# Kernel optimization log

Measured on AMD Instinct MI355X. Metric: run time of the kernel, lower is better.

The kernel has to match this reference:

```python
import jax, jax.numpy as jnp
import numpy as np

H = 128
R = 14
B = 2048
TYPES = ['operator', 'table', 'column', 'predicate', 'operation', 'literal', 'numeral']
SIZES = {'operator': 100000, 'table': 20000, 'column': 120000, 'predicate': 60000,
         'operation': 100000, 'literal': 50000, 'numeral': 50000}
FEAT = {'operator': 4, 'table': 2, 'column': 10, 'predicate': 4, 'operation': 8,
        'literal': 1, 'numeral': 1}
# (name, src_type, dst_type, num_edges), order matches edge_type_mapping in the torch module
EDGES = [('ei_scannedby', 'table', 'operator', 100000),
         ('ei_pred_filters', 'predicate', 'operator', 100000),
         ('ei_outputby', 'column', 'operator', 100000),
         ('ei_col_connects', 'column', 'operation', 100000),
         ('ei_calledby', 'operator', 'operator', 100000),
         ('ei_op_filters', 'operation', 'operator', 100000),
         ('ei_op_connects', 'operation', 'predicate', 100000),
         ('ei_lit_connects', 'literal', 'operation', 100000),
         ('ei_num_connects', 'numeral', 'operation', 100000),
         ('ei_lit_self', 'literal', 'literal', 50000),
         ('ei_num_self', 'numeral', 'numeral', 50000),
         ('ei_tab_self', 'table', 'table', 20000),
         ('ei_col_self', 'column', 'column', 120000),
         ('ei_pred_self', 'predicate', 'predicate', 60000)]
OFFS = {}
_o = 0
for _t in TYPES:
    OFFS[_t] = _o
    _o += SIZES[_t]
N_TOTAL = _o


def setup_inputs():
    key = jax.random.key(0)
    ks = iter(jax.random.split(key, 64))
    inp = {}
    for t in TYPES:
        inp['x_' + t] = jax.random.normal(next(ks), (SIZES[t], FEAT[t]), jnp.float32)
    for name, s, d, E in EDGES:
        src = jax.random.randint(next(ks), (E,), 0, SIZES[s], jnp.int32)
        dst = jax.random.randint(next(ks), (E,), 0, SIZES[d], jnp.int32)
        inp[name] = jnp.stack([src, dst])
    inp['batch_operator'] = jnp.sort(
        jax.random.randint(next(ks), (SIZES['operator'],), 0, B, jnp.int32))

    def lin_w(k, din, dout):
        s = 1.0 / float(np.sqrt(din))
        return jax.random.uniform(k, (din, dout), jnp.float32, -s, s)

    for t in TYPES:
        inp['W_' + t] = lin_w(next(ks), FEAT[t], H)
        inp['b_' + t] = jnp.zeros((H,), jnp.float32)
    for c in ('c1', 'c2'):
        inp[c + '_root'] = lin_w(next(ks), H, H)
        inp[c + '_rel'] = jax.random.normal(next(ks), (R, H, H), jnp.float32) / float(np.sqrt(H))
        inp[c + '_bias'] = jnp.zeros((H,), jnp.float32)
    inp['n1_g'] = jnp.ones((H,), jnp.float32); inp['n1_b'] = jnp.zeros((H,), jnp.float32)
    inp['n2_g'] = jnp.ones((H,), jnp.float32); inp['n2_b'] = jnp.zeros((H,), jnp.float32)
    inp['W_lin'] = lin_w(next(ks), H, 1)
    inp['b_lin'] = jnp.zeros((1,), jnp.float32)
    return inp


def layer_norm(x, g, b, eps=1e-5):
    mu = jnp.mean(x, axis=-1, keepdims=True)
    var = jnp.var(x, axis=-1, keepdims=True)
    return (x - mu) * jax.lax.rsqrt(var + eps) * g + b


def rgcn(x, rel_edges, w_root, w_rel, bias):
    # PyG RGCNConv: root transform + per-relation gather -> GEMM -> scatter-mean into dst
    out = x @ w_root
    for r, (src, dst) in enumerate(rel_edges):
        msg = x[src] @ w_rel[r]  # [E_r, H]
        agg = jax.ops.segment_sum(msg, dst, num_segments=N_TOTAL)
        cnt = jax.ops.segment_sum(jnp.ones(src.shape, x.dtype), dst, num_segments=N_TOTAL)
        out = out + agg / jnp.maximum(cnt, 1.0)[:, None]
    return out + bias


def reference(x_operator, x_table, x_column, x_predicate, x_operation, x_literal, x_numeral,
              ei_scannedby, ei_pred_filters, ei_outputby, ei_col_connects, ei_calledby,
              ei_op_filters, ei_op_connects, ei_lit_connects, ei_num_connects, ei_lit_self,
              ei_num_self, ei_tab_self, ei_col_self, ei_pred_self, batch_operator,
              W_operator, b_operator, W_table, b_table, W_column, b_column,
              W_predicate, b_predicate, W_operation, b_operation, W_literal, b_literal,
              W_numeral, b_numeral, c1_root, c1_rel, c1_bias, c2_root, c2_rel, c2_bias,
              n1_g, n1_b, n2_g, n2_b, W_lin, b_lin):
    # per-node-type input embedding, then concat in fixed type order
    x = jnp.concatenate([
        x_operator @ W_operator + b_operator,
        x_table @ W_table + b_table,
        x_column @ W_column + b_column,
        x_predicate @ W_predicate + b_predicate,
        x_operation @ W_operation + b_operation,
        x_literal @ W_literal + b_literal,
        x_numeral @ W_numeral + b_numeral], axis=0)
    eis = [ei_scannedby, ei_pred_filters, ei_outputby, ei_col_connects, ei_calledby,
           ei_op_filters, ei_op_connects, ei_lit_connects, ei_num_connects, ei_lit_self,
           ei_num_self, ei_tab_self, ei_col_self, ei_pred_self]
    rel_edges = [(e[0] + OFFS[s], e[1] + OFFS[d]) for e, (_, s, d, _) in zip(eis, EDGES)]
    h = rgcn(x, rel_edges, c1_root, c1_rel, c1_bias)
    h = layer_norm(jax.nn.elu(h), n1_g, n1_b)  # dropout is identity in eval mode
    h = rgcn(h, rel_edges, c2_root, c2_rel, c2_bias)
    h = layer_norm(jax.nn.elu(h), n2_g, n2_b)
    op = h[:SIZES['operator']]  # operator offset is 0
    cnt = jax.ops.segment_sum(jnp.ones((op.shape[0],), op.dtype), batch_operator, num_segments=B)
    pooled = jax.ops.segment_sum(op, batch_operator, num_segments=B) / jnp.maximum(cnt, 1.0)[:, None]
    return (pooled @ W_lin + b_lin)[:, 0]  # [B]
```

## Files before the change

kernel.cpp:

```cpp
#include <hip/hip_runtime.h>
#include <hip/hip_bf16.h>
#include <math.h>

#define HD 128
#define N_OP 100000
#define N_L1 400000
#define NB 2048
#define CNT_TOT 1160000
#define EDG_TOT 1100000

typedef short short8 __attribute__((ext_vector_type(8)));
typedef float floatx4 __attribute__((ext_vector_type(4)));

static const int REL_E[14]    = {100000,100000,100000,100000,100000,100000,100000,100000,100000,50000,50000,20000,120000,60000};
static const int REL_DSZ[14]  = {100000,100000,100000,100000,100000,100000,60000,100000,100000,50000,50000,20000,120000,60000};
static const int CNT_OFF[14]  = {0,100000,200000,300000,400000,500000,600000,660000,760000,860000,910000,960000,980000,1100000};
static const int SRC_T[14] = {1,3,2,2,0,4,4,5,6,5,6,1,2,3};
static const int TF[7]  = {4,2,10,4,8,1,1};
static const size_t AGR_OFF[14] = {0,200000,600000,1600000,2600000,3000000,3800000,4280000,4380000,0,0,4480000,4520000,5720000};
#define AGR_TOT 5960000
static const int RELW[14] = {4,7,12,93,23,28,70,104,106,-1,-1,40,54,79};
static const int RELI[14] = {6,11,22,103,27,36,78,105,107,-1,-1,42,64,83};
static const int ROOTW[5] = {0,38,44,66,85};
static const int ROOTB[5] = {37,43,65,84,108};
#define WL1_ROWS 109

__device__ inline unsigned short f2bf(float f) {
  union { float f; unsigned int u; } v; v.f = f;
  unsigned int r = v.u + 0x7FFF + ((v.u >> 16) & 1);
  return (unsigned short)(r >> 16);
}
__device__ inline float bfu2f(unsigned short u) {
  union { unsigned int i; float f; } v; v.i = ((unsigned int)u) << 16; return v.f;
}

struct CJob { const int* dst; int coff; int E; int blk0; };
struct CPackK { CJob j[12]; int bblk0; const int* batch; float* pcnt; int nop; };

__global__ void count_k(CPackK P, int* __restrict__ ICNT) {
  int b = blockIdx.x;
  if (b >= P.bblk0) {
    int i = (b - P.bblk0) * 256 + threadIdx.x;
    if (i < P.nop) atomicAdd(&P.pcnt[P.batch[i]], 1.0f);
    return;
  }
  int ji = 0;
#pragma unroll
  for (int i = 1; i < 12; ++i) if (b >= P.j[i].blk0) ji = i;
  CJob J = P.j[ji];
  int e = (b - J.blk0) * 256 + threadIdx.x;
  if (e < J.E) atomicAdd(&ICNT[J.coff + J.dst[e]], 1);
}

#define SCAN_BLK 1024
__global__ void scan1(const int* __restrict__ in, int* __restrict__ out,
                      int* __restrict__ bsum, int n) {
  __shared__ int sh[256];
  int t = threadIdx.x;
  int base = blockIdx.x * SCAN_BLK + t * 4;
  int v0 = 0, v1 = 0, v2 = 0, v3 = 0;
  if (base + 3 < n) { int4 q = *(const int4*)&in[base]; v0 = q.x; v1 = q.y; v2 = q.z; v3 = q.w; }
  else {
    if (base < n) v0 = in[base];
    if (base + 1 < n) v1 = in[base + 1];
    if (base + 2 < n) v2 = in[base + 2];
    if (base + 3 < n) v3 = in[base + 3];
  }
  int ts = v0 + v1 + v2 + v3;
  sh[t] = ts; __syncthreads();
  for (int o = 1; o < 256; o <<= 1) {
    int x = (t >= o) ? sh[t - o] : 0;
    __syncthreads();
    sh[t] += x;
    __syncthreads();
  }
  int excl = sh[t] - ts;
  if (base < n) out[base] = excl;
  if (base + 1 < n) out[base + 1] = excl + v0;
  if (base + 2 < n) out[base + 2] = excl + v0 + v1;
  if (base + 3 < n) out[base + 3] = excl + v0 + v1 + v2;
  if (t == 255) bsum[blockIdx.x] = sh[255];
}

__global__ void scan2(int* __restrict__ bs, int nb) {
  __shared__ int sh[256];
  int t = threadIdx.x;
  const int C = 5;
  int v[C]; int ts = 0;
#pragma unroll
  for (int i = 0; i < C; ++i) { int idx = t * C + i; v[i] = (idx < nb) ? bs[idx] : 0; ts += v[i]; }
  sh[t] = ts; __syncthreads();
  for (int o = 1; o < 256; o <<= 1) {
    int x = (t >= o) ? sh[t - o] : 0;
    __syncthreads();
    sh[t] += x;
    __syncthreads();
  }
  int run = sh[t] - ts;
#pragma unroll
  for (int i = 0; i < C; ++i) { int idx = t * C + i; if (idx < nb) bs[idx] = run; run += v[i]; }
}

__global__ void scan3(int* __restrict__ CUR, int2* __restrict__ OFF2,
                      const int* __restrict__ ICNT, const int* __restrict__ bs, int n) {
  int i = blockIdx.x * 256 + threadIdx.x;
  if (i < n) {
    int o = CUR[i] + bs[i >> 10];
    CUR[i] = o;
    OFF2[i] = make_int2(o, ICNT[i]);
  }
}

struct FJob { const int* src; const int* dst; int coff; int E; int blk0; };
struct FPackK { FJob j[12]; };

__global__ void fill_k(FPackK P, int* __restrict__ CUR, int* __restrict__ EDG) {
  int b = blockIdx.x;
  int ji = 0;
#pragma unroll
  for (int i = 1; i < 12; ++i) if (b >= P.j[i].blk0) ji = i;
  FJob J = P.j[ji];
  int e = (b - J.blk0) * 256 + threadIdx.x;
  if (e < J.E) {
    int pos = atomicAdd(&CUR[J.coff + J.dst[e]], 1);
    EDG[pos] = J.src[e];
  }
}

struct GJob { const float* x; float* agr; int coff; int D; int F; int blk0; };
struct GPack { GJob j[12]; };

template <int F>
__device__ inline void gathF(const float* __restrict__ x, float* __restrict__ agr,
                             const int* __restrict__ EDG, int2 oc, int d) {
  if (oc.y == 0) return;
  float s[F];
#pragma unroll
  for (int f = 0; f < F; ++f) s[f] = 0.f;
  for (int e = 0; e < oc.y; ++e) {
    int si = EDG[oc.x + e];
    const float* xp = &x[(size_t)si * F];
#pragma unroll
    for (int f = 0; f < F; ++f) s[f] += xp[f];
  }
  float rc = 1.0f / (float)oc.y;
  float* ap = &agr[(size_t)d * F];
#pragma unroll
  for (int f = 0; f < F; ++f) ap[f] = s[f] * rc;
}

__global__ void gather_all(GPack P, const int2* __restrict__ OFF2, const int* __restrict__ EDG) {
  int b = blockIdx.x;
  int ji = 0;
#pragma unroll
  for (int i = 1; i < 12; ++i) if (b >= P.j[i].blk0) ji = i;
  GJob J = P.j[ji];
  int d = (b - J.blk0) * 256 + threadIdx.x;
  if (d >= J.D) return;
  int2 oc = OFF2[J.coff + d];
  switch (J.F) {
    case 1:  gathF<1>(J.x, J.agr, EDG, oc, d); break;
    case 2:  gathF<2>(J.x, J.agr, EDG, oc, d); break;
    case 4:  gathF<4>(J.x, J.agr, EDG, oc, d); break;
    case 8:  gathF<8>(J.x, J.agr, EDG, oc, d); break;
    default: gathF<10>(J.x, J.agr, EDG, oc, d); break;
  }
}

struct CombJob { const float* A; const float* bin; const float* Mtx; const float* extra; float* Wout; float* bout; int F; };
struct CombPack { CombJob j[17]; };

__global__ void weights_prep(CombPack P, const float* __restrict__ c2root,
                             const float* __restrict__ c2rel, __hip_bfloat16* __restrict__ Wt) {
  int b = blockIdx.x;
  if (b < 17) {
    if (threadIdx.x >= 128) return;
    CombJob J = P.j[b];
    int c = threadIdx.x;
    for (int f = 0; f <= J.F; ++f) {
      const float* arow = (f < J.F) ? &J.A[f * HD] : J.bin;
      float s = (f < J.F) ? 0.f : (J.extra ? J.extra[c] : 0.f);
      for (int k = 0; k < HD; ++k) s = fmaf(arow[k], J.Mtx[k * HD + c], s);
      if (f < J.F) J.Wout[f * HD + c] = s;
      else J.bout[c] = s;
    }
  } else {
    const int RID[6] = {-1, 0, 1, 2, 4, 5};
    int j = b - 17;
    const float* W = (j == 0) ? c2root : (c2rel + (size_t)RID[j] * HD * HD);
    __hip_bfloat16* o = Wt + (size_t)j * HD * 136;
    for (int i = threadIdx.x; i < HD * HD; i += 256) {
      int k = i >> 7, n = i & 127;
      o[n * 136 + k] = __float2bfloat16(W[i]);
    }
  }
}

struct L1v2 {
  const float* x0; const float* x1; const float* x2; const float* x3; const float* x4;
  const float* AGR; const float* WL1; const int2* OFF2;
  const float* g; const float* b;
  unsigned short* Hb;
};

template <int F>
__device__ inline void ld_rel(float* s, const float* __restrict__ agr,
                              const int2* __restrict__ OFF2, int cb, int row) {
  int cnt = OFF2[cb + row].y;
  if (cnt > 0) {
    const float* ap = &agr[(size_t)row * F];
#pragma unroll
    for (int f = 0; f < F; ++f) s[f] = ap[f];
    s[F] = 1.f;
  } else {
#pragma unroll
    for (int f = 0; f <= F; ++f) s[f] = 0.f;
  }
}

template <int KT>
__device__ inline float2 l1_dot(const float* __restrict__ Ls, const float (&s)[KT], int c2) {
  float2 a;
  a.x = Ls[KT * 128 + c2];
  a.y = Ls[KT * 128 + c2 + 1];
#pragma unroll
  for (int k = 0; k < KT; ++k) {
    a.x = fmaf(s[k], Ls[k * 128 + c2], a.x);
    a.y = fmaf(s[k], Ls[k * 128 + c2 + 1], a.y);
  }
  return a;
}

__device__ inline void l1_fin(float2 a, int c2, const float* __restrict__ g,
                              const float* __restrict__ bb,
                              unsigned short* __restrict__ Hb, int orow) {
  a.x = (a.x > 0.f) ? a.x : (expf(a.x) - 1.f);
  a.y = (a.y > 0.f) ? a.y : (expf(a.y) - 1.f);
  float s = a.x + a.y, sq = a.x * a.x + a.y * a.y;
#pragma unroll
  for (int m = 32; m >= 1; m >>= 1) {
    s += __shfl_xor(s, m, 64);
    sq += __shfl_xor(sq, m, 64);
  }
  float mean = s * (1.0f / HD);
  float var = sq * (1.0f / HD) - mean * mean;
  float rstd = rsqrtf(var + 1e-5f);
  float2 gg = *(const float2*)&g[c2];
  float2 b2 = *(const float2*)&bb[c2];
  float ox = (a.x - mean) * rstd * gg.x + b2.x;
  float oy = (a.y - mean) * rstd * gg.y + b2.y;
  unsigned int pack = (unsigned int)f2bf(ox) | ((unsigned int)f2bf(oy) << 16);
  *(unsigned int*)&Hb[(size_t)orow * HD + c2] = pack;
}

__global__ __launch_bounds__(256) void layer1_v2(L1v2 A) {
  __shared__ float Ls[38 * 128];
  const int b = blockIdx.x, t = threadIdx.x;
  const int wv = t >> 6, lane = t & 63, c2 = lane * 2;
  int type, seg;
  if (b < 391) { type = 0; seg = b; }
  else if (b < 470) { type = 1; seg = b - 391; }
  else if (b < 939) { type = 2; seg = b - 470; }
  else if (b < 1174) { type = 3; seg = b - 939; }
  else { type = 4; seg = b - 1174; }
  const int NR[5] = {38, 6, 22, 19, 24};
  const int RB[5] = {0, 38, 44, 66, 85};
  const int TR[5] = {100000, 20000, 120000, 60000, 100000};
  const int OB[5] = {0, 100000, 120000, 240000, 300000};
  {
    const float4* src = (const float4*)(A.WL1 + RB[type] * 128);
    float4* dst = (float4*)Ls;
    int n4 = NR[type] * 32;
    for (int i = t; i < n4; i += 256) dst[i] = src[i];
  }
  __syncthreads();
  const int row0 = seg * 256, M = TR[type], ob = OB[type];

  if (type == 0) {
    for (int it = 0; it < 64; ++it) {
      int row = row0 + it * 4 + wv;
      if (row >= M) break;
      float s[37];
      const float* xp = &A.x0[(size_t)row * 4];
#pragma unroll
      for (int f = 0; f < 4; ++f) s[f] = xp[f];
      ld_rel<2>(s + 4, A.AGR + 0, A.OFF2, 0, row);
      ld_rel<4>(s + 7, A.AGR + 200000, A.OFF2, 100000, row);
      ld_rel<10>(s + 12, A.AGR + 600000, A.OFF2, 200000, row);
      ld_rel<4>(s + 23, A.AGR + 2600000, A.OFF2, 400000, row);
      ld_rel<8>(s + 28, A.AGR + 3000000, A.OFF2, 500000, row);
      l1_fin(l1_dot<37>(Ls, s, c2), c2, A.g, A.b, A.Hb, ob + row);
    }
  } else if (type == 1) {
    for (int it = 0; it < 64; ++it) {
      int row = row0 + it * 4 + wv;
      if (row >= M) break;
      float s[5];
      const float* xp = &A.x1[(size_t)row * 2];
#pragma unroll
      for (int f = 0; f < 2; ++f) s[f] = xp[f];
      ld_rel<2>(s + 2, A.AGR + 4480000, A.OFF2, 960000, row);
      l1_fin(l1_dot<5>(Ls, s, c2), c2, A.g, A.b, A.Hb, ob + row);
    }
  } else if (type == 2) {
    for (int it = 0; it < 64; ++it) {
      int row = row0 + it * 4 + wv;
      if (row >= M) break;
      float s[21];
      const float* xp = &A.x2[(size_t)row * 10];
#pragma unroll
      for (int f = 0; f < 10; ++f) s[f] = xp[f];
      ld_rel<10>(s + 10, A.AGR + 4520000, A.OFF2, 980000, row);
      l1_fin(l1_dot<21>(Ls, s, c2), c2, A.g, A.b, A.Hb, ob + row);
    }
  } else if (type == 3) {
    for (int it = 0; it < 64; ++it) {
      int row = row0 + it * 4 + wv;
      if (row >= M) break;
      float s[18];
      const float* xp = &A.x3[(size_t)row * 4];
#pragma unroll
      for (int f = 0; f < 4; ++f) s[f] = xp[f];
      ld_rel<8>(s + 4, A.AGR + 3800000, A.OFF2, 600000, row);
      ld_rel<4>(s + 13, A.AGR + 5720000, A.OFF2, 1100000, row);
      l1_fin(l1_dot<18>(Ls, s, c2), c2, A.g, A.b, A.Hb, ob + row);
    }
  } else {
    for (int it = 0; it < 64; ++it) {
      int row = row0 + it * 4 + wv;
      if (row >= M) break;
      float s[23];
      const float* xp = &A.x4[(size_t)row * 8];
#pragma unroll
      for (int f = 0; f < 8; ++f) s[f] = xp[f];
      ld_rel<10>(s + 8, A.AGR + 1600000, A.OFF2, 300000, row);
      ld_rel<1>(s + 19, A.AGR + 4280000, A.OFF2, 660000, row);
      ld_rel<1>(s + 21, A.AGR + 4380000, A.OFF2, 760000, row);
      l1_fin(l1_dot<23>(Ls, s, c2), c2, A.g, A.b, A.Hb, ob + row);
    }
  }
}

__global__ __launch_bounds__(256, 4)
void l2_fused(const unsigned short* __restrict__ Hb, const unsigned short* __restrict__ Wall,
              const int2* __restrict__ OFF2, const int* __restrict__ EDG,
              const float* __restrict__ c2bias, const float* __restrict__ n2g,
              const float* __restrict__ n2b, const float* __restrict__ Wl,
              const int* __restrict__ batch, float* __restrict__ accb, int M) {
  const int CSR_OFF[5] = {0, 100000, 200000, 400000, 500000};
  const int SOFF[5]    = {100000, 240000, 120000, 0, 300000};
  __shared__ unsigned short Ws[128 * 136];
  const int t = threadIdx.x, wv = t >> 6, ln = t & 63;
  const int quad = ln >> 4, ln15 = ln & 15, q8 = quad * 8;
  const int m0 = blockIdx.x * 64;
  const int rowA = m0 + wv * 16 + ln15;

  float bias_c[8], gw[8];
  float pg = 0.f, pb = 0.f;
#pragma unroll
  for (int nt = 0; nt < 8; ++nt) {
    int col = nt * 16 + ln15;
    float wl = Wl[col], gc = n2g[col], bc = n2b[col];
    bias_c[nt] = c2bias[col];
    gw[nt] = gc * wl;
    pg += gc * wl;
    pb += bc * wl;
  }
#pragma unroll
  for (int m = 8; m >= 1; m >>= 1) {
    pg += __shfl_xor(pg, m, 64);
    pb += __shfl_xor(pb, m, 64);
  }

  floatx4 acc[8];
#pragma unroll
  for (int b = 0; b < 8; ++b) acc[b] = (floatx4){0.f, 0.f, 0.f, 0.f};

  for (int term = 0; term < 6; ++term) {
    __syncthreads();
    {
      const uint4* wg = (const uint4*)(Wall + (size_t)term * 128 * 136);
      uint4* ws4 = (uint4*)Ws;
#pragma unroll
      for (int i = 0; i < 9; ++i) {
        int idx = i * 256 + t;
        if (idx < 2176) ws4[idx] = wg[idx];
      }
    }
    __syncthreads();

    short8 afr[4];
    if (term == 0) {
      if (rowA < M) {
#pragma unroll
        for (int k4 = 0; k4 < 4; ++k4)
          afr[k4] = *(const short8*)&Hb[(size_t)rowA * HD + k4 * 32 + q8];
      } else {
#pragma unroll
        for (int k4 = 0; k4 < 4; ++k4)
#pragma unroll
          for (int j = 0; j < 8; ++j) afr[k4][j] = 0;
      }
    } else {
      float sum[4][8];
#pragma unroll
      for (int k4 = 0; k4 < 4; ++k4)
#pragma unroll
        for (int j = 0; j < 8; ++j) sum[k4][j] = 0.f;
      if (rowA < M) {
        int2 oc = OFF2[CSR_OFF[term - 1] + rowA];
        if (oc.y > 0) {
          int so = SOFF[term - 1];
          for (int e = 0; e < oc.y; ++e) {
            size_t s = (size_t)(EDG[oc.x + e] + so);
#pragma unroll
            for (int k4 = 0; k4 < 4; ++k4) {
              short8 h = *(const short8*)&Hb[s * HD + k4 * 32 + q8];
#pragma unroll
              for (int j = 0; j < 8; ++j) sum[k4][j] += bfu2f((unsigned short)h[j]);
            }
          }
          float rc = 1.0f / (float)oc.y;
#pragma unroll
          for (int k4 = 0; k4 < 4; ++k4)
#pragma unroll
            for (int j = 0; j < 8; ++j) sum[k4][j] *= rc;
        }
      }
#pragma unroll
      for (int k4 = 0; k4 < 4; ++k4)
#pragma unroll
        for (int j = 0; j < 8; ++j) afr[k4][j] = (short)f2bf(sum[k4][j]);
    }

#pragma unroll
    for (int nt = 0; nt < 8; ++nt) {
      int wrow = nt * 16 + ln15;
      short8 b0 = *(const short8*)&Ws[wrow * 136 + 0 + q8];
      short8 b1 = *(const short8*)&Ws[wrow * 136 + 32 + q8];
      short8 b2 = *(const short8*)&Ws[wrow * 136 + 64 + q8];
      short8 b3 = *(const short8*)&Ws[wrow * 136 + 96 + q8];
      acc[nt] = __builtin_amdgcn_mfma_f32_16x16x32_bf16(afr[0], b0, acc[nt], 0, 0, 0);
      acc[nt] = __builtin_amdgcn_mfma_f32_16x16x32_bf16(afr[1], b1, acc[nt], 0, 0, 0);
      acc[nt] = __builtin_amdgcn_mfma_f32_16x16x32_bf16(afr[2], b2, acc[nt], 0, 0, 0);
      acc[nt] = __builtin_amdgcn_mfma_f32_16x16x32_bf16(afr[3], b3, acc[nt], 0, 0, 0);
    }
  }

#pragma unroll
  for (int r = 0; r < 4; ++r) {
    int rowD = m0 + wv * 16 + quad * 4 + r;
    float p = 0.f, q = 0.f, s1 = 0.f;
#pragma unroll
    for (int nt = 0; nt < 8; ++nt) {
      float v = acc[nt][r] + bias_c[nt];
      float e = (v > 0.f) ? v : (expf(v) - 1.f);
      p += e; q += e * e; s1 += e * gw[nt];
    }
#pragma unroll
    for (int m = 8; m >= 1; m >>= 1) {
      p += __shfl_xor(p, m, 64);
      q += __shfl_xor(q, m, 64);
      s1 += __shfl_xor(s1, m, 64);
    }
    if (ln15 == 0 && rowD < M) {
      float mean = p * (1.0f / HD);
      float var = q * (1.0f / HD) - mean * mean;
      float rstd = rsqrtf(var + 1e-5f);
      float o = rstd * (s1 - mean * pg) + pb;
      atomicAdd(&accb[batch[rowD]], o);
    }
  }
}

__global__ void final_kernel(const float* __restrict__ accb, const float* __restrict__ pcnt,
                             const float* __restrict__ bl, float* __restrict__ out) {
  int b = blockIdx.x * 256 + threadIdx.x;
  if (b < NB) out[b] = accb[b] / fmaxf(pcnt[b], 1.0f) + bl[0];
}

extern "C" void kernel_launch(void* const* d_in, const int* in_sizes, int n_in,
                              void* d_out, int out_size, void* d_ws, size_t ws_size,
                              hipStream_t stream) {
  const float* xt[7];
  for (int t = 0; t < 7; ++t) xt[t] = (const float*)d_in[t];
  const int* ei[14];
  for (int r = 0; r < 14; ++r) ei[r] = (const int*)d_in[7 + r];
  const int* batch = (const int*)d_in[21];
  const float* Wemb[7]; const float* bemb[7];
  for (int t = 0; t < 7; ++t) { Wemb[t] = (const float*)d_in[22 + 2 * t]; bemb[t] = (const float*)d_in[23 + 2 * t]; }
  const float* c_root[2] = {(const float*)d_in[36], (const float*)d_in[39]};
  const float* c_rel[2]  = {(const float*)d_in[37], (const float*)d_in[40]};
  const float* c_bias[2] = {(const float*)d_in[38], (const float*)d_in[41]};
  const float* ng[2] = {(const float*)d_in[42], (const float*)d_in[44]};
  const float* nbv[2] = {(const float*)d_in[43], (const float*)d_in[45]};
  const float* Wlin = (const float*)d_in[46];
  const float* blin = (const float*)d_in[47];
  float* out = (float*)d_out;

  char* base = (char*)d_ws;
  size_t off = 0;
  auto alloc = [&](size_t bytes) -> void* {
    void* p = base + off;
    off += (bytes + 255) & ~(size_t)255;
    return p;
  };
  __hip_bfloat16* Hb = (__hip_bfloat16*)alloc((size_t)N_L1 * HD * 2);
  float* AGR  = (float*)alloc((size_t)AGR_TOT * 4);
  int*   ICNT = (int*)alloc((size_t)CNT_TOT * 4);
  int*   CUR  = (int*)alloc((size_t)CNT_TOT * 4);
  int2*  OFF2 = (int2*)alloc((size_t)CNT_TOT * 8);
  int*   EDG  = (int*)alloc((size_t)EDG_TOT * 4);
  int*   BS   = (int*)alloc((size_t)1152 * 4);
  float* WL1  = (float*)alloc((size_t)WL1_ROWS * 128 * 4);
  __hip_bfloat16* WT2 = (__hip_bfloat16*)alloc((size_t)6 * HD * 136 * 2);
  float* ACC  = (float*)alloc((size_t)NB * 4);
  float* PCNT = (float*)alloc((size_t)NB * 4);

  static const int l1_rels[12] = {0,1,2,3,4,5,6,7,8,11,12,13};

  hipMemsetAsync(ICNT, 0, (size_t)CNT_TOT * 4, stream);
  hipMemsetAsync(ACC, 0, (size_t)2 * NB * 4, stream);

  CPackK CP1;
  int blk = 0;
  for (int q = 0; q < 12; ++q) {
    int r = l1_rels[q];
    CP1.j[q].dst = ei[r] + REL_E[r];
    CP1.j[q].coff = CNT_OFF[r];
    CP1.j[q].E = REL_E[r];
    CP1.j[q].blk0 = blk;
    blk += (REL_E[r] + 255) / 256;
  }
  CP1.bblk0 = blk; CP1.batch = batch; CP1.pcnt = PCNT; CP1.nop = N_OP;
  blk += (N_OP + 255) / 256;
  count_k<<<blk, 256, 0, stream>>>(CP1, ICNT);

  int nb1 = (CNT_TOT + SCAN_BLK - 1) / SCAN_BLK;
  scan1<<<nb1, 256, 0, stream>>>(ICNT, CUR, BS, CNT_TOT);
  scan2<<<1, 256, 0, stream>>>(BS, nb1);
  scan3<<<(CNT_TOT + 255) / 256, 256, 0, stream>>>(CUR, OFF2, ICNT, BS, CNT_TOT);

  FPackK FP;
  blk = 0;
  for (int q = 0; q < 12; ++q) {
    int r = l1_rels[q];
    FP.j[q].src = ei[r];
    FP.j[q].dst = ei[r] + REL_E[r];
    FP.j[q].coff = CNT_OFF[r];
    FP.j[q].E = REL_E[r];
    FP.j[q].blk0 = blk;
    blk += (REL_E[r] + 255) / 256;
  }
  fill_k<<<blk, 256, 0, stream>>>(FP, CUR, EDG);

  CombPack CP;
  for (int q = 0; q < 12; ++q) {
    int r = l1_rels[q]; int t = SRC_T[r];
    CombJob& J = CP.j[q];
    J.A = Wemb[t]; J.bin = bemb[t]; J.Mtx = c_rel[0] + (size_t)r * HD * HD;
    J.extra = nullptr;
    J.Wout = WL1 + (size_t)RELW[r] * 128;
    J.bout = WL1 + (size_t)RELI[r] * 128;
    J.F = TF[t];
  }
  for (int t = 0; t < 5; ++t) {
    CombJob& J = CP.j[12 + t];
    J.A = Wemb[t]; J.bin = bemb[t]; J.Mtx = c_root[0];
    J.extra = c_bias[0];
    J.Wout = WL1 + (size_t)ROOTW[t] * 128;
    J.bout = WL1 + (size_t)ROOTB[t] * 128;
    J.F = TF[t];
  }
  weights_prep<<<23, 256, 0, stream>>>(CP, c_root[1], c_rel[1], WT2);

  GPack GP;
  blk = 0;
  for (int q = 0; q < 12; ++q) {
    int r = l1_rels[q]; int t = SRC_T[r];
    GP.j[q].x = xt[t];
    GP.j[q].agr = AGR + AGR_OFF[r];
    GP.j[q].coff = CNT_OFF[r];
    GP.j[q].D = REL_DSZ[r];
    GP.j[q].F = TF[t];
    GP.j[q].blk0 = blk;
    blk += (REL_DSZ[r] + 255) / 256;
  }
  gather_all<<<blk, 256, 0, stream>>>(GP, OFF2, EDG);

  L1v2 A;
  A.x0 = xt[0]; A.x1 = xt[1]; A.x2 = xt[2]; A.x3 = xt[3]; A.x4 = xt[4];
  A.AGR = AGR; A.WL1 = WL1; A.OFF2 = OFF2;
  A.g = ng[0]; A.b = nbv[0]; A.Hb = (unsigned short*)Hb;
  layer1_v2<<<1565, 256, 0, stream>>>(A);

  l2_fused<<<(N_OP + 63) / 64, 256, 0, stream>>>(
      (const unsigned short*)Hb, (const unsigned short*)WT2,
      OFF2, EDG, c_bias[1], ng[1], nbv[1], Wlin, batch, ACC, N_OP);

  final_kernel<<<(NB + 255) / 256, 256, 0, stream>>>(ACC, PCNT, blin, out);
}
```

Before: 677.6 us.

## Remap layer1 so each 16-lane group handles one row with 8 columns per lane

Rewrites the layer-1 dense+ELU+LayerNorm kernel so each wave processes four rows at once, each row split across 16 lanes that each own 8 contiguous columns. It uses float4 LDS weight reads and a uint4 bf16 store, and shortens the shuffle reduction to 4 steps. Rows per block drop from 256 to 64, so the grid grows from 1565 to 6252 blocks. The aim is more memory-level parallelism on the per-row gathers and fewer LDS and shuffle instructions, at the cost of more registers per thread and the weight staging being repeated across more blocks.

```diff
diff --git a/kernel.cpp b/kernel.cpp
--- a/kernel.cpp
+++ b/kernel.cpp
@@ -219,50 +219,68 @@
 }
 
 template <int KT>
-__device__ inline float2 l1_dot(const float* __restrict__ Ls, const float (&s)[KT], int c2) {
-  float2 a;
-  a.x = Ls[KT * 128 + c2];
-  a.y = Ls[KT * 128 + c2 + 1];
+__device__ inline void l1_dot8(const float* __restrict__ Ls, const float (&s)[KT],
+                               int c8, float (&a)[8]) {
+  {
+    float4 w0 = *(const float4*)&Ls[KT * 128 + c8];
+    float4 w1 = *(const float4*)&Ls[KT * 128 + c8 + 4];
+    a[0] = w0.x; a[1] = w0.y; a[2] = w0.z; a[3] = w0.w;
+    a[4] = w1.x; a[5] = w1.y; a[6] = w1.z; a[7] = w1.w;
+  }
 #pragma unroll
   for (int k = 0; k < KT; ++k) {
-    a.x = fmaf(s[k], Ls[k * 128 + c2], a.x);
-    a.y = fmaf(s[k], Ls[k * 128 + c2 + 1], a.y);
-  }
-  return a;
-}
-
-__device__ inline void l1_fin(float2 a, int c2, const float* __restrict__ g,
-                              const float* __restrict__ bb,
-                              unsigned short* __restrict__ Hb, int orow) {
-  a.x = (a.x > 0.f) ? a.x : (expf(a.x) - 1.f);
-  a.y = (a.y > 0.f) ? a.y : (expf(a.y) - 1.f);
-  float s = a.x + a.y, sq = a.x * a.x + a.y * a.y;
-#pragma unroll
-  for (int m = 32; m >= 1; m >>= 1) {
-    s += __shfl_xor(s, m, 64);
-    sq += __shfl_xor(sq, m, 64);
-  }
-  float mean = s * (1.0f / HD);
-  float var = sq * (1.0f / HD) - mean * mean;
+    float4 w0 = *(const float4*)&Ls[k * 128 + c8];
+    float4 w1 = *(const float4*)&Ls[k * 128 + c8 + 4];
+    a[0] = fmaf(s[k], w0.x, a[0]); a[1] = fmaf(s[k], w0.y, a[1]);
+    a[2] = fmaf(s[k], w0.z, a[2]); a[3] = fmaf(s[k], w0.w, a[3]);
+    a[4] = fmaf(s[k], w1.x, a[4]); a[5] = fmaf(s[k], w1.y, a[5]);
+    a[6] = fmaf(s[k], w1.z, a[6]); a[7] = fmaf(s[k], w1.w, a[7]);
+  }
+}
+
+__device__ inline void l1_fin8(float (&a)[8], int c8, const float* __restrict__ g,
+                               const float* __restrict__ bb,
+                               unsigned short* __restrict__ Hb, int orow) {
+  float p = 0.f, q = 0.f;
+#pragma unroll
+  for (int j = 0; j < 8; ++j) {
+    a[j] = (a[j] > 0.f) ? a[j] : (expf(a[j]) - 1.f);
+    p += a[j]; q += a[j] * a[j];
+  }
+#pragma unroll
+  for (int m = 8; m >= 1; m >>= 1) {
+    p += __shfl_xor(p, m, 64);
+    q += __shfl_xor(q, m, 64);
+  }
+  float mean = p * (1.0f / HD);
+  float var = q * (1.0f / HD) - mean * mean;
   float rstd = rsqrtf(var + 1e-5f);
-  float2 gg = *(const float2*)&g[c2];
-  float2 b2 = *(const float2*)&bb[c2];
-  float ox = (a.x - mean) * rstd * gg.x + b2.x;
-  float oy = (a.y - mean) * rstd * gg.y + b2.y;
-  unsigned int pack = (unsigned int)f2bf(ox) | ((unsigned int)f2bf(oy) << 16);
-  *(unsigned int*)&Hb[(size_t)orow * HD + c2] = pack;
-}
-
-__global__ __launch_bounds__(256) void layer1_v2(L1v2 A) {
+  float4 g0 = *(const float4*)&g[c8], g1 = *(const float4*)&g[c8 + 4];
+  float4 b0 = *(const float4*)&bb[c8], b1 = *(const float4*)&bb[c8 + 4];
+  float gg[8] = {g0.x, g0.y, g0.z, g0.w, g1.x, g1.y, g1.z, g1.w};
+  float bv[8] = {b0.x, b0.y, b0.z, b0.w, b1.x, b1.y, b1.z, b1.w};
+  unsigned int pk[4];
+#pragma unroll
+  for (int j = 0; j < 4; ++j) {
+    float o0 = (a[2 * j] - mean) * rstd * gg[2 * j] + bv[2 * j];
+    float o1 = (a[2 * j + 1] - mean) * rstd * gg[2 * j + 1] + bv[2 * j + 1];
+    pk[j] = (unsigned int)f2bf(o0) | ((unsigned int)f2bf(o1) << 16);
+  }
+  uint4 st; st.x = pk[0]; st.y = pk[1]; st.z = pk[2]; st.w = pk[3];
+  *(uint4*)&Hb[(size_t)orow * HD + c8] = st;
+}
+
+__global__ __launch_bounds__(256) void layer1_v3(L1v2 A) {
   __shared__ float Ls[38 * 128];
   const int b = blockIdx.x, t = threadIdx.x;
-  const int wv = t >> 6, lane = t & 63, c2 = lane * 2;
+  const int wv = t >> 6, ln = t & 63;
+  const int sub = ln >> 4, c8 = (ln & 15) * 8;
   int type, seg;
-  if (b < 391) { type = 0; seg = b; }
-  else if (b < 470) { type = 1; seg = b - 391; }
-  else if (b < 939) { type = 2; seg = b - 470; }
-  else if (b < 1174) { type = 3; seg = b - 939; }
-  else { type = 4; seg = b - 1174; }
+  if (b < 1563) { type = 0; seg = b; }
+  else if (b < 1876) { type = 1; seg = b - 1563; }
+  else if (b < 3751) { type = 2; seg = b - 1876; }
+  else if (b < 4689) { type = 3; seg = b - 3751; }
+  else { type = 4; seg = b - 4689; }
   const int NR[5] = {38, 6, 22, 19, 24};
   const int RB[5] = {0, 38, 44, 66, 85};
   const int TR[5] = {100000, 20000, 120000, 60000, 100000};
@@ -274,12 +292,13 @@
     for (int i = t; i < n4; i += 256) dst[i] = src[i];
   }
   __syncthreads();
-  const int row0 = seg * 256, M = TR[type], ob = OB[type];
+  const int row0 = seg * 64, M = TR[type], ob = OB[type];
 
   if (type == 0) {
-    for (int it = 0; it < 64; ++it) {
-      int row = row0 + it * 4 + wv;
-      if (row >= M) break;
+#pragma unroll
+    for (int it = 0; it < 4; ++it) {
+      int row = row0 + it * 16 + wv * 4 + sub;
+      if (row >= M) continue;
       float s[37];
       const float* xp = &A.x0[(size_t)row * 4];
 #pragma unroll
@@ -289,46 +308,58 @@
       ld_rel<10>(s + 12, A.AGR + 600000, A.OFF2, 200000, row);
       ld_rel<4>(s + 23, A.AGR + 2600000, A.OFF2, 400000, row);
       ld_rel<8>(s + 28, A.AGR + 3000000, A.OFF2, 500000, row);
-      l1_fin(l1_dot<37>(Ls, s, c2), c2, A.g, A.b, A.Hb, ob + row);
+      float a[8];
+      l1_dot8<37>(Ls, s, c8, a);
+      l1_fin8(a, c8, A.g, A.b, A.Hb, ob + row);
     }
   } else if (type == 1) {
-    for (int it = 0; it < 64; ++it) {
-      int row = row0 + it * 4 + wv;
-      if (row >= M) break;
+#pragma unroll
+    for (int it = 0; it < 4; ++it) {
+      int row = row0 + it * 16 + wv * 4 + sub;
+      if (row >= M) continue;
       float s[5];
       const float* xp = &A.x1[(size_t)row * 2];
 #pragma unroll
       for (int f = 0; f < 2; ++f) s[f] = xp[f];
       ld_rel<2>(s + 2, A.AGR + 4480000, A.OFF2, 960000, row);
-      l1_fin(l1_dot<5>(Ls, s, c2), c2, A.g, A.b, A.Hb, ob + row);
+      float a[8];
+      l1_dot8<5>(Ls, s, c8, a);
+      l1_fin8(a, c8, A.g, A.b, A.Hb, ob + row);
     }
   } else if (type == 2) {
-    for (int it = 0; it < 64; ++it) {
-      int row = row0 + it * 4 + wv;
-      if (row >= M) break;
+#pragma unroll
+    for (int it = 0; it < 4; ++it) {
+      int row = row0 + it * 16 + wv * 4 + sub;
+      if (row >= M) continue;
       float s[21];
       const float* xp = &A.x2[(size_t)row * 10];
 #pragma unroll
       for (int f = 0; f < 10; ++f) s[f] = xp[f];
       ld_rel<10>(s + 10, A.AGR + 4520000, A.OFF2, 980000, row);
-      l1_fin(l1_dot<21>(Ls, s, c2), c2, A.g, A.b, A.Hb, ob + row);
+      float a[8];
+      l1_dot8<21>(Ls, s, c8, a);
+      l1_fin8(a, c8, A.g, A.b, A.Hb, ob + row);
     }
   } else if (type == 3) {
-    for (int it = 0; it < 64; ++it) {
-      int row = row0 + it * 4 + wv;
-      if (row >= M) break;
+#pragma unroll
+    for (int it = 0; it < 4; ++it) {
+      int row = row0 + it * 16 + wv * 4 + sub;
+      if (row >= M) continue;
       float s[18];
       const float* xp = &A.x3[(size_t)row * 4];
 #pragma unroll
       for (int f = 0; f < 4; ++f) s[f] = xp[f];
       ld_rel<8>(s + 4, A.AGR + 3800000, A.OFF2, 600000, row);
       ld_rel<4>(s + 13, A.AGR + 5720000, A.OFF2, 1100000, row);
-      l1_fin(l1_dot<18>(Ls, s, c2), c2, A.g, A.b, A.Hb, ob + row);
+      float a[8];
+      l1_dot8<18>(Ls, s, c8, a);
+      l1_fin8(a, c8, A.g, A.b, A.Hb, ob + row);
     }
   } else {
-    for (int it = 0; it < 64; ++it) {
-      int row = row0 + it * 4 + wv;
-      if (row >= M) break;
+#pragma unroll
+    for (int it = 0; it < 4; ++it) {
+      int row = row0 + it * 16 + wv * 4 + sub;
+      if (row >= M) continue;
       float s[23];
       const float* xp = &A.x4[(size_t)row * 8];
 #pragma unroll
@@ -336,7 +367,9 @@
       ld_rel<10>(s + 8, A.AGR + 1600000, A.OFF2, 300000, row);
       ld_rel<1>(s + 19, A.AGR + 4280000, A.OFF2, 660000, row);
       ld_rel<1>(s + 21, A.AGR + 4380000, A.OFF2, 760000, row);
-      l1_fin(l1_dot<23>(Ls, s, c2), c2, A.g, A.b, A.Hb, ob + row);
+      float a[8];
+      l1_dot8<23>(Ls, s, c8, a);
+      l1_fin8(a, c8, A.g, A.b, A.Hb, ob + row);
     }
   }
 }
@@ -592,7 +625,7 @@
   A.x0 = xt[0]; A.x1 = xt[1]; A.x2 = xt[2]; A.x3 = xt[3]; A.x4 = xt[4];
   A.AGR = AGR; A.WL1 = WL1; A.OFF2 = OFF2;
   A.g = ng[0]; A.b = nbv[0]; A.Hb = (unsigned short*)Hb;
-  layer1_v2<<<1565, 256, 0, stream>>>(A);
+  layer1_v3<<<6252, 256, 0, stream>>>(A);
 
   l2_fused<<<(N_OP + 63) / 64, 256, 0, stream>>>(
       (const unsigned short*)Hb, (const unsigned short*)WT2,
```

Measured after the change: 612.9 us. -9.5%, faster.
